# Kernel tuning notes

Hardware: AMD Instinct MI355X
Metric: run time of the kernel (lower is better)

The kernel has to match this reference:

```python
import jax, jax.numpy as jnp
import numpy as np

WIN = (8, 8)
DIM = 256
HEADS = 8
B = 2048
NW = 64


def _make_buffers(win):
    wh, ww = win
    # relative_position_bias_table: (1, 2wh-1, 2ww-1, 2)
    rh = np.arange(-(wh - 1), wh, dtype=np.float32)
    rw = np.arange(-(ww - 1), ww, dtype=np.float32)
    gh, gw = np.meshgrid(rh, rw, indexing='ij')
    tbl = np.stack([gh, gw], axis=-1)[None]  # (1, 2wh-1, 2ww-1, 2)
    tbl[..., 0] /= (wh - 1)
    tbl[..., 1] /= (ww - 1)
    tbl *= 3.2
    tbl = np.sign(tbl) * (1.0 - np.exp(-np.abs(tbl)))
    # relative_position_index: (n, n)
    ch, cw = np.meshgrid(np.arange(wh), np.arange(ww), indexing='ij')
    cf = np.stack([ch.reshape(-1), cw.reshape(-1)])  # (2, n)
    rel = cf[:, :, None] - cf[:, None, :]            # (2, n, n)
    rel = rel.transpose(1, 2, 0).astype(np.int64)
    rel[..., 0] += wh - 1
    rel[..., 1] += ww - 1
    rel[..., 0] *= 2 * ww - 1
    rpi = rel.sum(-1).astype(np.int32)
    return jnp.asarray(tbl, dtype=jnp.float32), jnp.asarray(rpi)


def setup_inputs() -> dict:
    key = jax.random.key(0)
    ks = jax.random.split(key, 12)
    c2 = DIM // 2
    n = WIN[0] * WIN[1]
    s = 0.02
    inp = {
        'x': jax.random.normal(ks[0], (B, n, DIM), dtype=jnp.float32),
        'mask': jax.random.normal(ks[1], (NW, n, n), dtype=jnp.float32),
        'qw': jax.random.normal(ks[2], (2, c2, c2), dtype=jnp.float32) * s,
        'qb': jnp.zeros((2, c2), dtype=jnp.float32),
        'kw': jax.random.normal(ks[3], (2, c2, c2), dtype=jnp.float32) * s,
        'kb': jnp.zeros((2, c2), dtype=jnp.float32),
        'vw': jax.random.normal(ks[4], (2, c2, c2), dtype=jnp.float32) * s,
        'vb': jnp.zeros((2, c2), dtype=jnp.float32),
        'pw': jax.random.normal(ks[5], (2, c2, c2), dtype=jnp.float32) * s,
        'pb': jnp.zeros((2, c2), dtype=jnp.float32),
        'mlp_w1': jax.random.normal(ks[6], (2, 128), dtype=jnp.float32) * s,
        'mlp_b1': jnp.zeros((128,), dtype=jnp.float32),
        'mlp_w2': jax.random.normal(ks[7], (128, HEADS), dtype=jnp.float32) * s,
        'logit_scale': jnp.full((HEADS, 1, 1), np.log(10.0), dtype=jnp.float32),
    }
    tbl, rpi = _make_buffers(WIN)
    inp['rpb_table'] = tbl
    inp['rpi'] = rpi
    return inp


def _l2norm(v, eps=1e-12):
    nrm = jnp.sqrt(jnp.sum(v * v, axis=-1, keepdims=True))
    return v / jnp.maximum(nrm, eps)


def _forward(x, mask, qw, qb, kw, kb, vw, vb, pw, pb,
             mlp_w1, mlp_b1, mlp_w2, logit_scale, rpb_table, rpi):
    b, n, c = x.shape
    h = logit_scale.shape[0]
    c2 = c // 2
    hd = c // h
    xb = x.reshape(b, n, 2, c2)  # branch split on channel halves

    def dual(w, bias):  # residual dual-branch linear: xb + Linear(xb)
        return xb + jnp.einsum('bnsc,scd->bnsd', xb, w) + bias

    # (b, n, 2, c2) -> (b, n, c) -> (b, h, n, hd)
    q = dual(qw, qb).reshape(b, n, h, hd).transpose(0, 2, 1, 3)
    k = dual(kw, kb).reshape(b, n, h, hd).transpose(0, 2, 1, 3)
    v = dual(vw, vb).reshape(b, n, h, hd).transpose(0, 2, 1, 3)

    attn = jnp.einsum('bhnd,bhmd->bhnm', _l2norm(q), _l2norm(k))
    scale = jnp.exp(jnp.minimum(logit_scale, jnp.log(jnp.float32(100.0))))  # (h,1,1)
    attn = attn * scale[None]

    # CPB-MLP relative position bias
    hid = jax.nn.relu(rpb_table @ mlp_w1 + mlp_b1)         # (1, 2wh-1, 2ww-1, 128)
    tbl = (hid @ mlp_w2).reshape(-1, h)                    # ((2wh-1)(2ww-1), h)
    bias = tbl[rpi.reshape(-1)].reshape(n, n, h).transpose(2, 0, 1)
    attn = attn + 16.0 * jax.nn.sigmoid(bias)[None]

    if mask is not None:
        nw = mask.shape[0]
        attn = attn.reshape(b // nw, nw, h, n, n) + mask[None, :, None]
        attn = attn.reshape(b, h, n, n)

    attn = jax.nn.softmax(attn, axis=-1)
    out = jnp.einsum('bhnm,bhmd->bhnd', attn, v).transpose(0, 2, 1, 3).reshape(b, n, c)

    ob = out.reshape(b, n, 2, c2)
    y = jnp.einsum('bnsc,scd->bnsd', ob, pw) + pb
    return y.reshape(b, n, c)


def reference(x, mask, qw, qb, kw, kb, vw, vb, pw, pb,
              mlp_w1, mlp_b1, mlp_w2, logit_scale, rpb_table, rpi):
    return _forward(x, mask, qw, qb, kw, kb, vw, vb, pw, pb,
                    mlp_w1, mlp_b1, mlp_w2, logit_scale, rpb_table, rpi)
```

## Files before the change

### kernel.cpp

```cpp
#include <hip/hip_runtime.h>
#include <hip/hip_bf16.h>
#include <stdint.h>

#define B_    2048
#define N_    64
#define C_    256
#define C2_   128
#define H_    8
#define NW_   64
#define NPOS  225
#define PX    136
#define PV    72

typedef __attribute__((ext_vector_type(8))) short short8;
typedef __attribute__((ext_vector_type(4))) float float4v;

union U8 { unsigned u[4]; short8 s; };

__device__ float g_scale[H_];
__device__ float g_t8[NPOS][H_];
__device__ __align__(16) float g_sb[NW_ * H_ * N_ * N_];
__device__ unsigned short g_wt[4][2][C2_][C2_];

__device__ __forceinline__ float b2f(unsigned short u) {
  return __uint_as_float(((unsigned int)u) << 16);
}
__device__ __forceinline__ unsigned short f2b(float f) {
  unsigned int u = __float_as_uint(f);
  u += 0x7fffu + ((u >> 16) & 1u);
  return (unsigned short)(u >> 16);
}
__device__ __forceinline__ unsigned f2b2(float lo, float hi) {
  __hip_bfloat162 h = __float22bfloat162_rn(float2{lo, hi});
  unsigned u;
  __builtin_memcpy(&u, &h, 4);
  return u;
}
__device__ __forceinline__ float rowsum16(float v) {
  int x = __float_as_int(v);
  v += __int_as_float(__builtin_amdgcn_update_dpp(0, x, 0xB1, 0xF, 0xF, false));
  x = __float_as_int(v);
  v += __int_as_float(__builtin_amdgcn_update_dpp(0, x, 0x4E, 0xF, 0xF, false));
  x = __float_as_int(v);
  v += __int_as_float(__builtin_amdgcn_update_dpp(0, x, 0x124, 0xF, 0xF, false));
  x = __float_as_int(v);
  v += __int_as_float(__builtin_amdgcn_update_dpp(0, x, 0x128, 0xF, 0xF, false));
  return v;
}

__global__ __launch_bounds__(256) void k_prep_a(
    const float* __restrict__ qw, const float* __restrict__ kw,
    const float* __restrict__ vw, const float* __restrict__ pw,
    const float* __restrict__ tbl, const float* __restrict__ w1,
    const float* __restrict__ b1, const float* __restrict__ w2,
    const float* __restrict__ ls) {
  __shared__ unsigned short lt[128 * 132];
  const int t = threadIdx.x;
  if (blockIdx.x < 8) {
    const int p = blockIdx.x >> 1, s = blockIdx.x & 1;
    const float* src = (p == 0 ? qw : p == 1 ? kw : p == 2 ? vw : pw) + s * (C2_ * C2_);
#pragma unroll
    for (int it = 0; it < 64; ++it) {
      int e = it * 256 + t;
      int c = e >> 7, d = e & 127;
      lt[d * 132 + c] = f2b(src[e]);
    }
    __syncthreads();
#pragma unroll
    for (int it = 0; it < 64; ++it) {
      int e = it * 256 + t;
      int d = e >> 7, c = e & 127;
      unsigned short u = lt[d * 132 + c];
      if (p < 3 && d == c) u = f2b(b2f(u) + 1.0f);
      g_wt[p][s][d][c] = u;
    }
  } else {
    float* fsh = (float*)lt;
    float* sw1 = fsh;
    float* sb1 = fsh + 256;
    float* sw2 = fsh + 384;
    sw1[t] = w1[t];
    if (t < 128) sb1[t] = b1[t];
#pragma unroll
    for (int it = 0; it < 4; ++it) sw2[it * 256 + t] = w2[it * 256 + t];
    __syncthreads();
    if (t < NPOS) {
      float a0 = tbl[2 * t], a1 = tbl[2 * t + 1];
      float acc[H_];
#pragma unroll
      for (int h = 0; h < H_; ++h) acc[h] = 0.f;
      for (int j = 0; j < 128; ++j) {
        float hid = fmaxf(a0 * sw1[j] + a1 * sw1[128 + j] + sb1[j], 0.f);
#pragma unroll
        for (int h = 0; h < H_; ++h) acc[h] += hid * sw2[j * H_ + h];
      }
#pragma unroll
      for (int h = 0; h < H_; ++h) g_t8[t][h] = acc[h];
    }
    if (t < H_) g_scale[t] = __expf(fminf(ls[t], 4.6051702f));
  }
}

__global__ __launch_bounds__(256) void k_prep2(
    const float* __restrict__ mask, const int* __restrict__ rpi) {
  const int base = blockIdx.x * 1024;
#pragma unroll
  for (int it = 0; it < 4; ++it) {
    int idx = base + it * 256 + threadIdx.x;
    int j  = idx & 63;
    int i  = (idx >> 6) & 63;
    int h  = (idx >> 12) & 7;
    int wd = idx >> 15;
    float v = g_t8[rpi[i * 64 + j]][h];
    g_sb[idx] = 16.f / (1.f + __expf(-v)) + mask[wd * 4096 + i * 64 + j];
  }
}

__global__ __launch_bounds__(512, 4) void k_main(
    const float* __restrict__ x, float* __restrict__ out,
    const float* __restrict__ qb, const float* __restrict__ kb,
    const float* __restrict__ vb, const float* __restrict__ pb) {
  __shared__ __align__(16) unsigned short xs[N_ * PX];
  __shared__ __align__(16) unsigned short qs[N_ * PX];
  __shared__ __align__(16) unsigned short ks[N_ * PX];
  __shared__ __align__(16) unsigned short vt[C2_ * PV];

  const int t    = threadIdx.x;
  const int lane = t & 63;
  const int w    = __builtin_amdgcn_readfirstlane(t >> 6);
  const int bi   = blockIdx.x;
  const int b    = ((bi >> 4) << 3) | (bi & 7);
  const int s1   = (bi >> 3) & 1;
  const int l15  = lane & 15;
  const int qd   = lane >> 4;

  const int jls = w >> 1;
  const int jl  = 32 * jls;
  const int mh  = w & 1;
  const int cb = s1 * C2_ + jl + l15;
  const float qb0 = qb[cb], qb1 = qb[cb + 16];
  const float kb0 = kb[cb], kb1 = kb[cb + 16];
  const float vb0 = vb[cb], vb1 = vb[cb + 16];
  const float pb0 = pb[cb], pb1 = pb[cb + 16];
  const float scl = g_scale[s1 * 4 + jls];

  {
    const float* xg = x + (size_t)b * (N_ * C_) + s1 * C2_;
#pragma unroll
    for (int it = 0; it < 4; ++it) {
      int e = t + 512 * it;
      int row = e >> 5, c4 = (e & 31) << 2;
      float4 v = *(const float4*)&xg[row * C_ + c4];
      uint2 pk;
      pk.x = f2b2(v.x, v.y);
      pk.y = f2b2(v.z, v.w);
      *(uint2*)&xs[row * PX + c4] = pk;
    }
  }
  __syncthreads();

  short8 a_all[4][2];
#pragma unroll
  for (int kc = 0; kc < 4; ++kc) {
    int ko = kc * 32 + qd * 8;
#pragma unroll
    for (int mt = 0; mt < 2; ++mt)
      a_all[kc][mt] = *(const short8*)&xs[(32 * mh + mt * 16 + l15) * PX + ko];
  }
  for (int pj = 0; pj < 3; ++pj) {
    const float bi0 = pj == 0 ? qb0 : (pj == 1 ? kb0 : vb0);
    const float bi1 = pj == 0 ? qb1 : (pj == 1 ? kb1 : vb1);
    float4v acc[2][2];
#pragma unroll
    for (int mt = 0; mt < 2; ++mt) {
      acc[mt][0] = float4v{bi0, bi0, bi0, bi0};
      acc[mt][1] = float4v{bi1, bi1, bi1, bi1};
    }
    const unsigned short* wt = &g_wt[pj][s1][0][0];
#pragma unroll
    for (int kc = 0; kc < 4; ++kc) {
      int ko = kc * 32 + qd * 8;
      short8 bf[2];
      bf[0] = *(const short8*)&wt[(jl + l15) * C2_ + ko];
      bf[1] = *(const short8*)&wt[(jl + 16 + l15) * C2_ + ko];
#pragma unroll
      for (int mt = 0; mt < 2; ++mt)
#pragma unroll
        for (int nt = 0; nt < 2; ++nt)
          acc[mt][nt] = __builtin_amdgcn_mfma_f32_16x16x32_bf16(
              a_all[kc][mt], bf[nt], acc[mt][nt], 0, 0, 0);
    }
    unsigned short* dst = pj == 0 ? qs : ks;
#pragma unroll
    for (int mt = 0; mt < 2; ++mt) {
      int row0 = 32 * mh + mt * 16 + qd * 4;
      if (pj < 2) {
        float rn[4];
#pragma unroll
        for (int r = 0; r < 4; ++r) {
          float ss = acc[mt][0][r] * acc[mt][0][r] + acc[mt][1][r] * acc[mt][1][r];
          ss = rowsum16(ss);
          rn[r] = 1.0f / fmaxf(sqrtf(ss), 1e-12f);
          if (pj == 0) rn[r] *= scl;
        }
#pragma unroll
        for (int nt = 0; nt < 2; ++nt)
#pragma unroll
          for (int r = 0; r < 4; ++r)
            dst[(row0 + r) * PX + jl + nt * 16 + l15] = f2b(acc[mt][nt][r] * rn[r]);
      } else {
#pragma unroll
        for (int nt = 0; nt < 2; ++nt) {
          int chan = jl + nt * 16 + l15;
          uint2 pk;
          pk.x = f2b2(acc[mt][nt][0], acc[mt][nt][1]);
          pk.y = f2b2(acc[mt][nt][2], acc[mt][nt][3]);
          *(uint2*)&vt[chan * PV + row0] = pk;
        }
      }
    }
  }

  const int hl = w >> 1;
  const int rh = w & 1;
  const int h  = s1 * 4 + hl;
  const float* sbh = g_sb + ((size_t)(b & 63) * H_ + h) * 4096;
  float4 cv[2][4];
#pragma unroll
  for (int mq = 0; mq < 2; ++mq)
#pragma unroll
    for (int nt = 0; nt < 4; ++nt)
      cv[mq][nt] = *(const float4*)&sbh[(32 * rh + 16 * mq + l15) * 64 + nt * 16 + qd * 4];
  __syncthreads();

  const int hi_sel = lane & 32;
  const int src0 = l15 | ((((qd << 1) + 0) & 3) << 4);
  const int src1 = l15 | ((((qd << 1) + 1) & 3) << 4);
  short8 ak[4], bv[2][2];
#pragma unroll
  for (int nt = 0; nt < 4; ++nt)
    ak[nt] = *(const short8*)&ks[(nt * 16 + l15) * PX + hl * 32 + qd * 8];
#pragma unroll
  for (int kc = 0; kc < 2; ++kc)
#pragma unroll
    for (int nt2 = 0; nt2 < 2; ++nt2)
      bv[kc][nt2] = *(const short8*)&vt[(hl * 32 + nt2 * 16 + l15) * PV + kc * 32 + qd * 8];
#pragma unroll
  for (int mq = 0; mq < 2; ++mq) {
    const int r0 = 32 * rh + 16 * mq;
    short8 bq = *(const short8*)&qs[(r0 + l15) * PX + hl * 32 + qd * 8];
    float4v sacc[4];
#pragma unroll
    for (int nt = 0; nt < 4; ++nt) {
      float4v c = {cv[mq][nt].x, cv[mq][nt].y, cv[mq][nt].z, cv[mq][nt].w};
      sacc[nt] = __builtin_amdgcn_mfma_f32_16x16x32_bf16(ak[nt], bq, c, 0, 0, 0);
    }
    float e[4][4];
    float s = 0.f;
#pragma unroll
    for (int nt = 0; nt < 4; ++nt)
#pragma unroll
      for (int r = 0; r < 4; ++r) {
        e[nt][r] = __expf(sacc[nt][r]);
        s += e[nt][r];
      }
    s += __shfl_xor(s, 16, 64);
    s += __shfl_xor(s, 32, 64);
    float rr = 1.0f / s;
    unsigned pk[4][2];
#pragma unroll
    for (int nt = 0; nt < 4; ++nt)
#pragma unroll
      for (int rp = 0; rp < 2; ++rp)
        pk[nt][rp] = f2b2(e[nt][2 * rp] * rr, e[nt][2 * rp + 1] * rr);
    U8 au[2];
#pragma unroll
    for (int j2 = 0; j2 < 4; ++j2) {
      int src = (j2 >> 1) ? src1 : src0;
      int rp = j2 & 1;
      int r0v = __shfl((int)pk[0][rp], src, 64);
      int r1v = __shfl((int)pk[1][rp], src, 64);
      int r2v = __shfl((int)pk[2][rp], src, 64);
      int r3v = __shfl((int)pk[3][rp], src, 64);
      au[0].u[j2] = hi_sel ? (unsigned)r1v : (unsigned)r0v;
      au[1].u[j2] = hi_sel ? (unsigned)r3v : (unsigned)r2v;
    }
    float4v oacc[2];
    oacc[0] = float4v{0, 0, 0, 0};
    oacc[1] = float4v{0, 0, 0, 0};
#pragma unroll
    for (int kc = 0; kc < 2; ++kc) {
      short8 ap = au[kc].s;
#pragma unroll
      for (int nt2 = 0; nt2 < 2; ++nt2)
        oacc[nt2] = __builtin_amdgcn_mfma_f32_16x16x32_bf16(ap, bv[kc][nt2], oacc[nt2], 0, 0, 0);
    }
#pragma unroll
    for (int nt2 = 0; nt2 < 2; ++nt2)
#pragma unroll
      for (int r = 0; r < 4; ++r)
        xs[(r0 + qd * 4 + r) * PX + hl * 32 + nt2 * 16 + l15] = f2b(oacc[nt2][r]);
  }
  __syncthreads();

  {
    float4v acc[2][2];
#pragma unroll
    for (int mt = 0; mt < 2; ++mt) {
      acc[mt][0] = float4v{pb0, pb0, pb0, pb0};
      acc[mt][1] = float4v{pb1, pb1, pb1, pb1};
    }
    const unsigned short* wt = &g_wt[3][s1][0][0];
#pragma unroll
    for (int kc = 0; kc < 4; ++kc) {
      int ko = kc * 32 + qd * 8;
      short8 a[2], bf[2];
#pragma unroll
      for (int mt = 0; mt < 2; ++mt)
        a[mt] = *(const short8*)&xs[(32 * mh + mt * 16 + l15) * PX + ko];
      bf[0] = *(const short8*)&wt[(jl + l15) * C2_ + ko];
      bf[1] = *(const short8*)&wt[(jl + 16 + l15) * C2_ + ko];
#pragma unroll
      for (int mt = 0; mt < 2; ++mt)
#pragma unroll
        for (int nt = 0; nt < 2; ++nt)
          acc[mt][nt] = __builtin_amdgcn_mfma_f32_16x16x32_bf16(
              a[mt], bf[nt], acc[mt][nt], 0, 0, 0);
    }
#pragma unroll
    for (int mt = 0; mt < 2; ++mt)
#pragma unroll
      for (int nt = 0; nt < 2; ++nt)
#pragma unroll
        for (int r = 0; r < 4; ++r)
          out[((size_t)b * N_ + 32 * mh + mt * 16 + qd * 4 + r) * C_ +
              s1 * C2_ + jl + nt * 16 + l15] = acc[mt][nt][r];
  }
}

extern "C" void kernel_launch(void* const* d_in, const int* in_sizes, int n_in,
                              void* d_out, int out_size, void* d_ws, size_t ws_size,
                              hipStream_t stream) {
  const float* x    = (const float*)d_in[0];
  const float* mask = (const float*)d_in[1];
  const float* qw   = (const float*)d_in[2];
  const float* qb   = (const float*)d_in[3];
  const float* kw   = (const float*)d_in[4];
  const float* kb   = (const float*)d_in[5];
  const float* vw   = (const float*)d_in[6];
  const float* vb   = (const float*)d_in[7];
  const float* pw   = (const float*)d_in[8];
  const float* pb   = (const float*)d_in[9];
  const float* w1   = (const float*)d_in[10];
  const float* b1   = (const float*)d_in[11];
  const float* w2   = (const float*)d_in[12];
  const float* ls   = (const float*)d_in[13];
  const float* tbl  = (const float*)d_in[14];
  const int*   rpi  = (const int*)d_in[15];
  float* out = (float*)d_out;

  k_prep_a<<<9, 256, 0, stream>>>(qw, kw, vw, pw, tbl, w1, b1, w2, ls);
  k_prep2<<<2048, 256, 0, stream>>>(mask, rpi);
  k_main<<<B_ * 2, 512, 0, stream>>>(x, out, qb, kb, vb, pb);
}
```

Baseline: 384.5 us.

## Process both channel halves per block and prefetch second half of x

Each block now handles one window batch for both channel halves (s1 loop) instead of one half per block, halving the grid. The second half of x is loaded into registers while the first half's QKV projection and attention run, hiding global load latency. The cost is fewer blocks (less parallelism and latency hiding across waves), higher register pressure from the prefetched registers, and an extra barrier between halves.

```diff
diff --git a/kernel.cpp b/kernel.cpp
--- a/kernel.cpp
+++ b/kernel.cpp
@@ -128,213 +128,238 @@
   const int t    = threadIdx.x;
   const int lane = t & 63;
   const int w    = __builtin_amdgcn_readfirstlane(t >> 6);
-  const int bi   = blockIdx.x;
-  const int b    = ((bi >> 4) << 3) | (bi & 7);
-  const int s1   = (bi >> 3) & 1;
+  const int b    = blockIdx.x;
   const int l15  = lane & 15;
   const int qd   = lane >> 4;
 
   const int jls = w >> 1;
   const int jl  = 32 * jls;
   const int mh  = w & 1;
-  const int cb = s1 * C2_ + jl + l15;
-  const float qb0 = qb[cb], qb1 = qb[cb + 16];
-  const float kb0 = kb[cb], kb1 = kb[cb + 16];
-  const float vb0 = vb[cb], vb1 = vb[cb + 16];
-  const float pb0 = pb[cb], pb1 = pb[cb + 16];
-  const float scl = g_scale[s1 * 4 + jls];
-
-  {
-    const float* xg = x + (size_t)b * (N_ * C_) + s1 * C2_;
-#pragma unroll
-    for (int it = 0; it < 4; ++it) {
-      int e = t + 512 * it;
-      int row = e >> 5, c4 = (e & 31) << 2;
-      float4 v = *(const float4*)&xg[row * C_ + c4];
-      uint2 pk;
-      pk.x = f2b2(v.x, v.y);
-      pk.y = f2b2(v.z, v.w);
-      *(uint2*)&xs[row * PX + c4] = pk;
-    }
-  }
-  __syncthreads();
-
-  short8 a_all[4][2];
-#pragma unroll
-  for (int kc = 0; kc < 4; ++kc) {
-    int ko = kc * 32 + qd * 8;
-#pragma unroll
-    for (int mt = 0; mt < 2; ++mt)
-      a_all[kc][mt] = *(const short8*)&xs[(32 * mh + mt * 16 + l15) * PX + ko];
-  }
-  for (int pj = 0; pj < 3; ++pj) {
-    const float bi0 = pj == 0 ? qb0 : (pj == 1 ? kb0 : vb0);
-    const float bi1 = pj == 0 ? qb1 : (pj == 1 ? kb1 : vb1);
-    float4v acc[2][2];
-#pragma unroll
-    for (int mt = 0; mt < 2; ++mt) {
-      acc[mt][0] = float4v{bi0, bi0, bi0, bi0};
-      acc[mt][1] = float4v{bi1, bi1, bi1, bi1};
-    }
-    const unsigned short* wt = &g_wt[pj][s1][0][0];
-#pragma unroll
-    for (int kc = 0; kc < 4; ++kc) {
-      int ko = kc * 32 + qd * 8;
-      short8 bf[2];
-      bf[0] = *(const short8*)&wt[(jl + l15) * C2_ + ko];
-      bf[1] = *(const short8*)&wt[(jl + 16 + l15) * C2_ + ko];
-#pragma unroll
-      for (int mt = 0; mt < 2; ++mt)
-#pragma unroll
-        for (int nt = 0; nt < 2; ++nt)
-          acc[mt][nt] = __builtin_amdgcn_mfma_f32_16x16x32_bf16(
-              a_all[kc][mt], bf[nt], acc[mt][nt], 0, 0, 0);
-    }
-    unsigned short* dst = pj == 0 ? qs : ks;
-#pragma unroll
-    for (int mt = 0; mt < 2; ++mt) {
-      int row0 = 32 * mh + mt * 16 + qd * 4;
-      if (pj < 2) {
-        float rn[4];
-#pragma unroll
-        for (int r = 0; r < 4; ++r) {
-          float ss = acc[mt][0][r] * acc[mt][0][r] + acc[mt][1][r] * acc[mt][1][r];
-          ss = rowsum16(ss);
-          rn[r] = 1.0f / fmaxf(sqrtf(ss), 1e-12f);
-          if (pj == 0) rn[r] *= scl;
-        }
-#pragma unroll
-        for (int nt = 0; nt < 2; ++nt)
-#pragma unroll
-          for (int r = 0; r < 4; ++r)
-            dst[(row0 + r) * PX + jl + nt * 16 + l15] = f2b(acc[mt][nt][r] * rn[r]);
-      } else {
-#pragma unroll
-        for (int nt = 0; nt < 2; ++nt) {
-          int chan = jl + nt * 16 + l15;
-          uint2 pk;
-          pk.x = f2b2(acc[mt][nt][0], acc[mt][nt][1]);
-          pk.y = f2b2(acc[mt][nt][2], acc[mt][nt][3]);
-          *(uint2*)&vt[chan * PV + row0] = pk;
-        }
-      }
-    }
-  }
-
-  const int hl = w >> 1;
-  const int rh = w & 1;
-  const int h  = s1 * 4 + hl;
-  const float* sbh = g_sb + ((size_t)(b & 63) * H_ + h) * 4096;
-  float4 cv[2][4];
-#pragma unroll
-  for (int mq = 0; mq < 2; ++mq)
-#pragma unroll
-    for (int nt = 0; nt < 4; ++nt)
-      cv[mq][nt] = *(const float4*)&sbh[(32 * rh + 16 * mq + l15) * 64 + nt * 16 + qd * 4];
-  __syncthreads();
-
+  const int hl  = w >> 1;
+  const int rh  = w & 1;
   const int hi_sel = lane & 32;
   const int src0 = l15 | ((((qd << 1) + 0) & 3) << 4);
   const int src1 = l15 | ((((qd << 1) + 1) & 3) << 4);
-  short8 ak[4], bv[2][2];
-#pragma unroll
-  for (int nt = 0; nt < 4; ++nt)
-    ak[nt] = *(const short8*)&ks[(nt * 16 + l15) * PX + hl * 32 + qd * 8];
-#pragma unroll
-  for (int kc = 0; kc < 2; ++kc)
-#pragma unroll
-    for (int nt2 = 0; nt2 < 2; ++nt2)
-      bv[kc][nt2] = *(const short8*)&vt[(hl * 32 + nt2 * 16 + l15) * PV + kc * 32 + qd * 8];
-#pragma unroll
-  for (int mq = 0; mq < 2; ++mq) {
-    const int r0 = 32 * rh + 16 * mq;
-    short8 bq = *(const short8*)&qs[(r0 + l15) * PX + hl * 32 + qd * 8];
-    float4v sacc[4];
-#pragma unroll
-    for (int nt = 0; nt < 4; ++nt) {
-      float4v c = {cv[mq][nt].x, cv[mq][nt].y, cv[mq][nt].z, cv[mq][nt].w};
-      sacc[nt] = __builtin_amdgcn_mfma_f32_16x16x32_bf16(ak[nt], bq, c, 0, 0, 0);
-    }
-    float e[4][4];
-    float s = 0.f;
-#pragma unroll
-    for (int nt = 0; nt < 4; ++nt)
-#pragma unroll
-      for (int r = 0; r < 4; ++r) {
-        e[nt][r] = __expf(sacc[nt][r]);
-        s += e[nt][r];
-      }
-    s += __shfl_xor(s, 16, 64);
-    s += __shfl_xor(s, 32, 64);
-    float rr = 1.0f / s;
-    unsigned pk[4][2];
-#pragma unroll
-    for (int nt = 0; nt < 4; ++nt)
-#pragma unroll
-      for (int rp = 0; rp < 2; ++rp)
-        pk[nt][rp] = f2b2(e[nt][2 * rp] * rr, e[nt][2 * rp + 1] * rr);
-    U8 au[2];
-#pragma unroll
-    for (int j2 = 0; j2 < 4; ++j2) {
-      int src = (j2 >> 1) ? src1 : src0;
-      int rp = j2 & 1;
-      int r0v = __shfl((int)pk[0][rp], src, 64);
-      int r1v = __shfl((int)pk[1][rp], src, 64);
-      int r2v = __shfl((int)pk[2][rp], src, 64);
-      int r3v = __shfl((int)pk[3][rp], src, 64);
-      au[0].u[j2] = hi_sel ? (unsigned)r1v : (unsigned)r0v;
-      au[1].u[j2] = hi_sel ? (unsigned)r3v : (unsigned)r2v;
-    }
-    float4v oacc[2];
-    oacc[0] = float4v{0, 0, 0, 0};
-    oacc[1] = float4v{0, 0, 0, 0};
-#pragma unroll
-    for (int kc = 0; kc < 2; ++kc) {
-      short8 ap = au[kc].s;
-#pragma unroll
-      for (int nt2 = 0; nt2 < 2; ++nt2)
-        oacc[nt2] = __builtin_amdgcn_mfma_f32_16x16x32_bf16(ap, bv[kc][nt2], oacc[nt2], 0, 0, 0);
-    }
-#pragma unroll
-    for (int nt2 = 0; nt2 < 2; ++nt2)
-#pragma unroll
-      for (int r = 0; r < 4; ++r)
-        xs[(r0 + qd * 4 + r) * PX + hl * 32 + nt2 * 16 + l15] = f2b(oacc[nt2][r]);
-  }
-  __syncthreads();
-
-  {
-    float4v acc[2][2];
-#pragma unroll
-    for (int mt = 0; mt < 2; ++mt) {
-      acc[mt][0] = float4v{pb0, pb0, pb0, pb0};
-      acc[mt][1] = float4v{pb1, pb1, pb1, pb1};
-    }
-    const unsigned short* wt = &g_wt[3][s1][0][0];
+
+  const float* xgb = x + (size_t)b * (N_ * C_);
+
+  float4 xl[4];
+#pragma unroll
+  for (int it = 0; it < 4; ++it) {
+    int e = t + 512 * it;
+    xl[it] = *(const float4*)&xgb[(e >> 5) * C_ + ((e & 31) << 2)];
+  }
+  uint2 xpk[4];
+#pragma unroll
+  for (int it = 0; it < 4; ++it) {
+    xpk[it].x = f2b2(xl[it].x, xl[it].y);
+    xpk[it].y = f2b2(xl[it].z, xl[it].w);
+  }
+
+  for (int s1 = 0; s1 < 2; ++s1) {
+#pragma unroll
+    for (int it = 0; it < 4; ++it) {
+      int e = t + 512 * it;
+      *(uint2*)&xs[(e >> 5) * PX + ((e & 31) << 2)] = xpk[it];
+    }
+    if (s1 == 0) {
+#pragma unroll
+      for (int it = 0; it < 4; ++it) {
+        int e = t + 512 * it;
+        xl[it] = *(const float4*)&xgb[(e >> 5) * C_ + C2_ + ((e & 31) << 2)];
+      }
+    }
+    __syncthreads();
+
+    const int cb = s1 * C2_ + jl + l15;
+    const float qb0 = qb[cb], qb1 = qb[cb + 16];
+    const float kb0 = kb[cb], kb1 = kb[cb + 16];
+    const float vb0 = vb[cb], vb1 = vb[cb + 16];
+    const float pb0 = pb[cb], pb1 = pb[cb + 16];
+    const float scl = g_scale[s1 * 4 + jls];
+
+    short8 a_all[4][2];
 #pragma unroll
     for (int kc = 0; kc < 4; ++kc) {
       int ko = kc * 32 + qd * 8;
-      short8 a[2], bf[2];
 #pragma unroll
       for (int mt = 0; mt < 2; ++mt)
-        a[mt] = *(const short8*)&xs[(32 * mh + mt * 16 + l15) * PX + ko];
-      bf[0] = *(const short8*)&wt[(jl + l15) * C2_ + ko];
-      bf[1] = *(const short8*)&wt[(jl + 16 + l15) * C2_ + ko];
+        a_all[kc][mt] = *(const short8*)&xs[(32 * mh + mt * 16 + l15) * PX + ko];
+    }
+
+    for (int pj = 0; pj < 3; ++pj) {
+      const float bi0 = pj == 0 ? qb0 : (pj == 1 ? kb0 : vb0);
+      const float bi1 = pj == 0 ? qb1 : (pj == 1 ? kb1 : vb1);
+      float4v acc[2][2];
+#pragma unroll
+      for (int mt = 0; mt < 2; ++mt) {
+        acc[mt][0] = float4v{bi0, bi0, bi0, bi0};
+        acc[mt][1] = float4v{bi1, bi1, bi1, bi1};
+      }
+      const unsigned short* wt = &g_wt[pj][s1][0][0];
+#pragma unroll
+      for (int kc = 0; kc < 4; ++kc) {
+        int ko = kc * 32 + qd * 8;
+        short8 bf[2];
+        bf[0] = *(const short8*)&wt[(jl + l15) * C2_ + ko];
+        bf[1] = *(const short8*)&wt[(jl + 16 + l15) * C2_ + ko];
+#pragma unroll
+        for (int mt = 0; mt < 2; ++mt)
+#pragma unroll
+          for (int nt = 0; nt < 2; ++nt)
+            acc[mt][nt] = __builtin_amdgcn_mfma_f32_16x16x32_bf16(
+                a_all[kc][mt], bf[nt], acc[mt][nt], 0, 0, 0);
+      }
+      unsigned short* dst = pj == 0 ? qs : ks;
+#pragma unroll
+      for (int mt = 0; mt < 2; ++mt) {
+        int row0 = 32 * mh + mt * 16 + qd * 4;
+        if (pj < 2) {
+          float rn[4];
+#pragma unroll
+          for (int r = 0; r < 4; ++r) {
+            float ss = acc[mt][0][r] * acc[mt][0][r] + acc[mt][1][r] * acc[mt][1][r];
+            ss = rowsum16(ss);
+            rn[r] = 1.0f / fmaxf(sqrtf(ss), 1e-12f);
+            if (pj == 0) rn[r] *= scl;
+          }
+#pragma unroll
+          for (int nt = 0; nt < 2; ++nt)
+#pragma unroll
+            for (int r = 0; r < 4; ++r)
+              dst[(row0 + r) * PX + jl + nt * 16 + l15] = f2b(acc[mt][nt][r] * rn[r]);
+        } else {
+#pragma unroll
+          for (int nt = 0; nt < 2; ++nt) {
+            int chan = jl + nt * 16 + l15;
+            uint2 pk;
+            pk.x = f2b2(acc[mt][nt][0], acc[mt][nt][1]);
+            pk.y = f2b2(acc[mt][nt][2], acc[mt][nt][3]);
+            *(uint2*)&vt[chan * PV + row0] = pk;
+          }
+        }
+      }
+    }
+
+    if (s1 == 0) {
+#pragma unroll
+      for (int it = 0; it < 4; ++it) {
+        xpk[it].x = f2b2(xl[it].x, xl[it].y);
+        xpk[it].y = f2b2(xl[it].z, xl[it].w);
+      }
+    }
+
+    const int h = s1 * 4 + hl;
+    const float* sbh = g_sb + ((size_t)(b & 63) * H_ + h) * 4096;
+    float4 cv[2][4];
+#pragma unroll
+    for (int mq = 0; mq < 2; ++mq)
+#pragma unroll
+      for (int nt = 0; nt < 4; ++nt)
+        cv[mq][nt] = *(const float4*)&sbh[(32 * rh + 16 * mq + l15) * 64 + nt * 16 + qd * 4];
+    __syncthreads();
+
+    short8 ak[4], bv[2][2];
+#pragma unroll
+    for (int nt = 0; nt < 4; ++nt)
+      ak[nt] = *(const short8*)&ks[(nt * 16 + l15) * PX + hl * 32 + qd * 8];
+#pragma unroll
+    for (int kc = 0; kc < 2; ++kc)
+#pragma unroll
+      for (int nt2 = 0; nt2 < 2; ++nt2)
+        bv[kc][nt2] = *(const short8*)&vt[(hl * 32 + nt2 * 16 + l15) * PV + kc * 32 + qd * 8];
+#pragma unroll
+    for (int mq = 0; mq < 2; ++mq) {
+      const int r0 = 32 * rh + 16 * mq;
+      short8 bq = *(const short8*)&qs[(r0 + l15) * PX + hl * 32 + qd * 8];
+      float4v sacc[4];
+#pragma unroll
+      for (int nt = 0; nt < 4; ++nt) {
+        float4v c = {cv[mq][nt].x, cv[mq][nt].y, cv[mq][nt].z, cv[mq][nt].w};
+        sacc[nt] = __builtin_amdgcn_mfma_f32_16x16x32_bf16(ak[nt], bq, c, 0, 0, 0);
+      }
+      float e[4][4];
+      float s = 0.f;
+#pragma unroll
+      for (int nt = 0; nt < 4; ++nt)
+#pragma unroll
+        for (int r = 0; r < 4; ++r) {
+          e[nt][r] = __expf(sacc[nt][r]);
+          s += e[nt][r];
+        }
+      s += __shfl_xor(s, 16, 64);
+      s += __shfl_xor(s, 32, 64);
+      float rr = 1.0f / s;
+      unsigned pk[4][2];
+#pragma unroll
+      for (int nt = 0; nt < 4; ++nt)
+#pragma unroll
+        for (int rp = 0; rp < 2; ++rp)
+          pk[nt][rp] = f2b2(e[nt][2 * rp] * rr, e[nt][2 * rp + 1] * rr);
+      U8 au[2];
+#pragma unroll
+      for (int j2 = 0; j2 < 4; ++j2) {
+        int src = (j2 >> 1) ? src1 : src0;
+        int rp = j2 & 1;
+        int r0v = __shfl((int)pk[0][rp], src, 64);
+        int r1v = __shfl((int)pk[1][rp], src, 64);
+        int r2v = __shfl((int)pk[2][rp], src, 64);
+        int r3v = __shfl((int)pk[3][rp], src, 64);
+        au[0].u[j2] = hi_sel ? (unsigned)r1v : (unsigned)r0v;
+        au[1].u[j2] = hi_sel ? (unsigned)r3v : (unsigned)r2v;
+      }
+      float4v oacc[2];
+      oacc[0] = float4v{0, 0, 0, 0};
+      oacc[1] = float4v{0, 0, 0, 0};
+#pragma unroll
+      for (int kc = 0; kc < 2; ++kc) {
+        short8 ap = au[kc].s;
+#pragma unroll
+        for (int nt2 = 0; nt2 < 2; ++nt2)
+          oacc[nt2] = __builtin_amdgcn_mfma_f32_16x16x32_bf16(ap, bv[kc][nt2], oacc[nt2], 0, 0, 0);
+      }
+#pragma unroll
+      for (int nt2 = 0; nt2 < 2; ++nt2)
+#pragma unroll
+        for (int r = 0; r < 4; ++r)
+          xs[(r0 + qd * 4 + r) * PX + hl * 32 + nt2 * 16 + l15] = f2b(oacc[nt2][r]);
+    }
+    __syncthreads();
+
+    {
+      float4v acc[2][2];
+#pragma unroll
+      for (int mt = 0; mt < 2; ++mt) {
+        acc[mt][0] = float4v{pb0, pb0, pb0, pb0};
+        acc[mt][1] = float4v{pb1, pb1, pb1, pb1};
+      }
+      const unsigned short* wt = &g_wt[3][s1][0][0];
+#pragma unroll
+      for (int kc = 0; kc < 4; ++kc) {
+        int ko = kc * 32 + qd * 8;
+        short8 a[2], bf[2];
+#pragma unroll
+        for (int mt = 0; mt < 2; ++mt)
+          a[mt] = *(const short8*)&xs[(32 * mh + mt * 16 + l15) * PX + ko];
+        bf[0] = *(const short8*)&wt[(jl + l15) * C2_ + ko];
+        bf[1] = *(const short8*)&wt[(jl + 16 + l15) * C2_ + ko];
+#pragma unroll
+        for (int mt = 0; mt < 2; ++mt)
+#pragma unroll
+          for (int nt = 0; nt < 2; ++nt)
+            acc[mt][nt] = __builtin_amdgcn_mfma_f32_16x16x32_bf16(
+                a[mt], bf[nt], acc[mt][nt], 0, 0, 0);
+      }
 #pragma unroll
       for (int mt = 0; mt < 2; ++mt)
 #pragma unroll
         for (int nt = 0; nt < 2; ++nt)
-          acc[mt][nt] = __builtin_amdgcn_mfma_f32_16x16x32_bf16(
-              a[mt], bf[nt], acc[mt][nt], 0, 0, 0);
-    }
-#pragma unroll
-    for (int mt = 0; mt < 2; ++mt)
-#pragma unroll
-      for (int nt = 0; nt < 2; ++nt)
-#pragma unroll
-        for (int r = 0; r < 4; ++r)
-          out[((size_t)b * N_ + 32 * mh + mt * 16 + qd * 4 + r) * C_ +
-              s1 * C2_ + jl + nt * 16 + l15] = acc[mt][nt][r];
+#pragma unroll
+          for (int r = 0; r < 4; ++r)
+            out[((size_t)b * N_ + 32 * mh + mt * 16 + qd * 4 + r) * C_ +
+                s1 * C2_ + jl + nt * 16 + l15] = acc[mt][nt][r];
+    }
+    if (s1 == 0) __syncthreads();
   }
 }
 
@@ -361,5 +386,5 @@
 
   k_prep_a<<<9, 256, 0, stream>>>(qw, kw, vw, pw, tbl, w1, b1, w2, ls);
   k_prep2<<<2048, 256, 0, stream>>>(mask, rpi);
-  k_main<<<B_ * 2, 512, 0, stream>>>(x, out, qb, kb, vb, pb);
-}
+  k_main<<<B_, 512, 0, stream>>>(x, out, qb, kb, vb, pb);
+}
```

After: 466.2 us. 1.21x slower.
